# Performance work log

Hardware: AMD Instinct MI355X
Metric: run time of the kernel (lower is better)

## Reference

```python
import jax, jax.numpy as jnp
import numpy as np
import math

SQRT32 = math.sqrt(32.0)


def _l2norm(x, eps=1e-12):
    # matches torch.nn.functional.normalize(dim=-1): x / max(||x||, eps)
    n = jnp.linalg.norm(x, axis=-1, keepdims=True)
    return x / jnp.maximum(n, eps)


def setup_inputs() -> dict:
    key = jax.random.key(0)
    k1, k2 = jax.random.split(key)
    z = jax.random.normal(k1, (8, 256, 32, 32), dtype=jnp.float32)
    # trunc_normal_(std=0.02) init approximated by scaled normal
    embed_weight = jax.random.normal(k2, (16384, 256), dtype=jnp.float32) * 0.02
    return {"z": z, "embed_weight": embed_weight}


def reference(z, embed_weight):
    # z: [b, d, h, w] channel-first -> pack to [b*h*w, d]
    b, d, h, w = z.shape
    zf = jnp.transpose(z, (0, 2, 3, 1)).reshape(-1, d)  # [N, d]

    # l2_norm=True, no predefined codebook: distance = -z @ normalize(E)^T
    ew = _l2norm(embed_weight)                          # [K, d]
    dist = -(zf @ ew.T)                                 # [N, K]
    min_encoding_indices = jnp.argmin(dist, axis=1)     # [N]

    # gather UNnormalized embedding rows, then normalize (as in source)
    z_q = _l2norm(embed_weight[min_encoding_indices])   # [N, d]

    # straight-through estimator
    z_q = zf + jax.lax.stop_gradient(z_q - zf)

    loss = jnp.zeros((1,), dtype=z.dtype)

    # unpack to [b, h, w, d]
    zq_bhwd = z_q.reshape(b, h, w, d)
    # torch .long() truncates toward zero; astype(int) does the same
    bit_indices = (zq_bhwd * SQRT32).astype(jnp.int32) + 4
    zq_out = jnp.transpose(zq_bhwd, (0, 3, 1, 2))       # [b, d, h, w]

    return zq_out, min_encoding_indices, bit_indices, loss
```

## Files before the change

### kernel.cpp

```cpp
#include <hip/hip_runtime.h>
#include <math.h>

#define D      256
#define K      16384
#define NPTS   8192
#define DELTA  0.2f
#define LCAP   1024
#define MAXCAP 4000000u

#define O_IDX  2097152
#define O_BIT  2105344
#define O_LOSS 4202496

typedef __attribute__((ext_vector_type(8))) short bf16x8;
typedef __attribute__((ext_vector_type(4))) float f32x4;
typedef unsigned long long u64;

__device__ __forceinline__ unsigned f2s(float f) {
    unsigned u = __float_as_uint(f);
    return (u & 0x80000000u) ? ~u : (u | 0x80000000u);
}
__device__ __forceinline__ float s2f(unsigned s) {
    return __uint_as_float((s & 0x80000000u) ? (s & 0x7fffffffu) : ~s);
}
__device__ __forceinline__ unsigned short f2bf(float f) {
    unsigned u = __float_as_uint(f);
    u += 0x7fffu + ((u >> 16) & 1u);
    return (unsigned short)(u >> 16);
}


__global__ __launch_bounds__(256) void prep(const float* __restrict__ E,
                                            const float* __restrict__ z,
                                            float* __restrict__ den,
                                            unsigned short* __restrict__ ewbT,
                                            unsigned short* __restrict__ zfbT,
                                            float* __restrict__ zf32,
                                            unsigned* __restrict__ gmax,
                                            u64* __restrict__ keys,
                                            unsigned* __restrict__ cnt) {
    const int blk = blockIdx.x, tid = threadIdx.x;
    if (blk < 512) {
        const int lane = tid & 63, wave = tid >> 6;
        if (blk < 32)        gmax[blk * 256 + tid] = 0u;
        else if (blk < 64)   keys[(blk - 32) * 256 + tid] = 0ull;
        else if (blk == 64 && tid < 2) cnt[tid] = 0u;
        #pragma unroll
        for (int j = 0; j < 8; ++j) {
            const int row = blk * 32 + wave * 8 + j;
            const float4 v = *(const float4*)(E + (size_t)row * D + lane * 4);
            float ss = v.x * v.x + v.y * v.y + v.z * v.z + v.w * v.w;
            #pragma unroll
            for (int o = 1; o < 64; o <<= 1) ss += __shfl_xor(ss, o);
            const float dn = fmaxf(sqrtf(ss), 1e-12f);
            const unsigned lo = (unsigned)f2bf(v.x / dn) | ((unsigned)f2bf(v.y / dn) << 16);
            const unsigned hi = (unsigned)f2bf(v.z / dn) | ((unsigned)f2bf(v.w / dn) << 16);
            *(uint2*)(ewbT + ((size_t)(lane >> 1) * K + row) * 8 + (lane & 1) * 4)
                = make_uint2(lo, hi);
            if (lane == 0) den[row] = dn;
        }
    } else {
        const int bi = blk - 512;
        const int b = bi >> 4, hw0 = (bi & 15) * 64;
        __shared__ float t[64][65];
        for (int dc = 0; dc < D; dc += 64) {
            #pragma unroll
            for (int it = 0; it < 16; ++it) {
                const int idx = it * 256 + tid;
                const int dl = idx >> 6, hw = idx & 63;
                t[dl][hw] = z[(size_t)(b * 256 + dc + dl) * 1024 + hw0 + hw];
            }
            __syncthreads();
            #pragma unroll
            for (int it = 0; it < 16; ++it) {
                const int idx = it * 256 + tid;
                const int pl = idx >> 6, dl = idx & 63;
                const float v = t[dl][pl];
                const int p = b * 1024 + hw0 + pl, k = dc + dl;
                zfbT[((size_t)(k >> 3) * NPTS + p) * 8 + (k & 7)] = f2bf(v);
                zf32[(size_t)p * D + k] = v;
            }
            __syncthreads();
        }
    }
}

#define GEMM_CORE()                                                                 \
    f32x4 acc[4][4];                                                                \
    _Pragma("unroll")                                                               \
    for (int i = 0; i < 4; ++i)                                                     \
        _Pragma("unroll")                                                           \
        for (int j = 0; j < 4; ++j) acc[i][j] = (f32x4){0.f, 0.f, 0.f, 0.f};        \
    {                                                                               \
        const unsigned short* pA = zfbT + ((size_t)quad * NPTS + m0 + wm * 64 + col) * 8; \
        const unsigned short* pB = ewbT + ((size_t)quad * K    + n0 + wn * 64 + col) * 8; \
        _Pragma("unroll")                                                           \
        for (int dc = 0; dc < 8; ++dc) {                                            \
            bf16x8 af[4], bfr[4];                                                   \
            _Pragma("unroll")                                                       \
            for (int mt = 0; mt < 4; ++mt)                                          \
                af[mt] = *(const bf16x8*)(pA + (size_t)dc * 4 * NPTS * 8 + mt * 128);\
            _Pragma("unroll")                                                       \
            for (int nt = 0; nt < 4; ++nt)                                          \
                bfr[nt] = *(const bf16x8*)(pB + (size_t)dc * 4 * K * 8 + nt * 128); \
            _Pragma("unroll")                                                       \
            for (int mt = 0; mt < 4; ++mt)                                          \
                _Pragma("unroll")                                                   \
                for (int nt = 0; nt < 4; ++nt)                                      \
                    acc[mt][nt] = __builtin_amdgcn_mfma_f32_16x16x32_bf16(af[mt], bfr[nt], \
                                                                          acc[mt][nt], 0, 0, 0); \
        }                                                                           \
    }

__global__ __launch_bounds__(256, 3) void score_seed(const unsigned short* __restrict__ zfbT,
                                                     const unsigned short* __restrict__ ewbT,
                                                     unsigned* __restrict__ gmax,
                                                     u64* __restrict__ cand,
                                                     unsigned* __restrict__ cnt,
                                                     unsigned cap) {
    __shared__ unsigned thrS[128];
    __shared__ u64 lbuf[LCAP];
    __shared__ unsigned lcount, lbase;

    const int tid = threadIdx.x, lane = tid & 63, wave = tid >> 6;
    const int quad = lane >> 4, col = lane & 15;
    const int wm = wave >> 1, wn = wave & 1;
    const int m0 = blockIdx.x * 128;
    const int n0 = blockIdx.y * 128;
    const int shsrc = lane & 48;

    if (tid < 128) thrS[tid] = 0u;
    if (tid == 0) lcount = 0u;

    GEMM_CORE()
    __syncthreads();

    float red[4][4];
    #pragma unroll
    for (int mt = 0; mt < 4; ++mt)
        #pragma unroll
        for (int r = 0; r < 4; ++r)
            red[mt][r] = fmaxf(fmaxf(acc[mt][0][r], acc[mt][1][r]),
                               fmaxf(acc[mt][2][r], acc[mt][3][r]));
    #pragma unroll
    for (int off = 1; off < 16; off <<= 1)
        #pragma unroll
        for (int mt = 0; mt < 4; ++mt)
            #pragma unroll
            for (int r = 0; r < 4; ++r)
                red[mt][r] = fmaxf(red[mt][r], __shfl_xor(red[mt][r], off));
    #pragma unroll
    for (int mt = 0; mt < 4; ++mt)
        #pragma unroll
        for (int r = 0; r < 4; ++r) {
            const int pl = wm * 64 + mt * 16 + quad * 4 + r;
            unsigned cur = 0;
            if (col == 0) {
                const unsigned enc = f2s(red[mt][r]);
                const unsigned old = atomicMax(&thrS[pl], enc);
                cur = old > enc ? old : enc;
            }
            cur = (unsigned)__shfl((int)cur, shsrc);
            red[mt][r] = s2f(cur) - DELTA;
        }

    const int ncode0 = n0 + wn * 64 + col;
    #pragma unroll
    for (int mt = 0; mt < 4; ++mt) {
        #pragma unroll
        for (int r = 0; r < 4; ++r) {
            const float tp = red[mt][r];
            const unsigned pt = m0 + wm * 64 + mt * 16 + quad * 4 + r;
            #pragma unroll
            for (int nt = 0; nt < 4; ++nt) {
                const float v = acc[mt][nt][r];
                if (v >= tp) {
                    const unsigned slot = atomicAdd(&lcount, 1u);
                    const u64 e = ((u64)((pt << 14) | (unsigned)(ncode0 + nt * 16)) << 32)
                                  | f2s(v);
                    if (slot < LCAP) lbuf[slot] = e;
                    else {
                        const unsigned g = atomicAdd(cnt, 1u);
                        if (g < cap) cand[g] = e;
                    }
                }
            }
        }
    }

    __syncthreads();
    if (tid < 128) atomicMax(&gmax[m0 + tid], thrS[tid]);
    const unsigned m_ = lcount < LCAP ? lcount : LCAP;
    if (tid == 0) lbase = atomicAdd(cnt, m_);
    __syncthreads();
    for (unsigned i = tid; i < m_; i += 256) {
        const unsigned g = lbase + i;
        if (g < cap) cand[g] = lbuf[i];
    }
}

__global__ __launch_bounds__(256, 3) void score_main(const unsigned short* __restrict__ zfbT,
                                                     const unsigned short* __restrict__ ewbT,
                                                     const unsigned* __restrict__ gmax,
                                                     u64* __restrict__ cand,
                                                     unsigned* __restrict__ cnt,
                                                     unsigned cap) {
    __shared__ float thrL[128];
    __shared__ u64 lbuf[LCAP];
    __shared__ unsigned lcount, lbase;

    const int tid = threadIdx.x, lane = tid & 63, wave = tid >> 6;
    const int quad = lane >> 4, col = lane & 15;
    const int wm = wave >> 1, wn = wave & 1;
    const int m0 = blockIdx.x * 128;
    const int n0 = (16 + blockIdx.y) * 128;

    if (tid < 128) thrL[tid] = s2f(gmax[m0 + tid]) - DELTA;
    if (tid == 0) lcount = 0u;

    GEMM_CORE()
    __syncthreads();

    const int ncode0 = n0 + wn * 64 + col;
    #pragma unroll
    for (int mt = 0; mt < 4; ++mt) {
        #pragma unroll
        for (int r = 0; r < 4; ++r) {
            const int pl = wm * 64 + mt * 16 + quad * 4 + r;
            const float tp = thrL[pl];
            #pragma unroll
            for (int nt = 0; nt < 4; ++nt) {
                const float v = acc[mt][nt][r];
                if (v >= tp) {
                    const unsigned slot = atomicAdd(&lcount, 1u);
                    const u64 e = ((u64)(((unsigned)pl + m0) << 14 | (unsigned)(ncode0 + nt * 16)) << 32)
                                  | f2s(v);
                    if (slot < LCAP) lbuf[slot] = e;
                    else {
                        const unsigned g = atomicAdd(cnt, 1u);
                        if (g < cap) cand[g] = e;
                    }
                }
            }
        }
    }

    __syncthreads();
    const unsigned m_ = lcount < LCAP ? lcount : LCAP;
    if (tid == 0) lbase = atomicAdd(cnt, m_);
    __syncthreads();
    for (unsigned i = tid; i < m_; i += 256) {
        const unsigned g = lbase + i;
        if (g < cap) cand[g] = lbuf[i];
    }
}

__global__ __launch_bounds__(256) void cand_max(const u64* __restrict__ cand,
                                                const unsigned* __restrict__ cnt,
                                                unsigned* __restrict__ gmax,
                                                unsigned cap) {
    const unsigned total = min(cnt[0], cap);
    const unsigned stride = gridDim.x * 256;
    for (unsigned i = blockIdx.x * 256 + threadIdx.x; i < total; i += stride) {
        const u64 e = cand[i];
        atomicMax(&gmax[(unsigned)(e >> 46)], (unsigned)(e & 0xffffffffull));
    }
}

__global__ __launch_bounds__(256) void rescore(const float* __restrict__ zf32,
                                               const float* __restrict__ E,
                                               const float* __restrict__ den,
                                               const unsigned* __restrict__ gmax,
                                               const u64* __restrict__ cand,
                                               const unsigned* __restrict__ cnt,
                                               u64* __restrict__ keys,
                                               unsigned cap) {
    const unsigned total = min(cnt[0], cap);
    const int lane = threadIdx.x & 63;
    const unsigned w = (blockIdx.x * 256 + threadIdx.x) >> 6;
    const unsigned nw = gridDim.x * 4;
    for (unsigned base = w * 64; base < total; base += nw * 64) {
        const unsigned i = base + lane;
        u64 e = 0;
        bool keep = false;
        if (i < total) {
            e = cand[i];
            const int p = (int)(e >> 46);
            keep = (s2f((unsigned)(e & 0xffffffffull)) >= s2f(gmax[p]) - DELTA);
        }
        u64 mask = __ballot(keep);
        while (mask) {
            const int src = __ffsll((long long)mask) - 1;
            mask &= mask - 1;
            const unsigned pc = (unsigned)__shfl((int)(unsigned)(e >> 32), src);
            const int p = pc >> 14, c = pc & 16383;
            const float dinv = 1.0f / den[c];
            const float4 a = *(const float4*)(zf32 + (size_t)p * D + lane * 4);
            const float4 b = *(const float4*)(E + (size_t)c * D + lane * 4);
            float sv = fmaf(a.x, b.x * dinv, fmaf(a.y, b.y * dinv,
                       fmaf(a.z, b.z * dinv, a.w * (b.w * dinv))));
            #pragma unroll
            for (int o = 1; o < 64; o <<= 1) sv += __shfl_xor(sv, o);
            if (lane == 0)
                atomicMax(keys + p, ((u64)f2s(sv) << 32) | (unsigned)(16383 - c));
        }
    }
}

__global__ __launch_bounds__(256) void finalize(const float* __restrict__ E,
                                                const float* __restrict__ den,
                                                const u64* __restrict__ keys,
                                                float* __restrict__ out) {
    __shared__ float t[32][257];
    __shared__ int sIdx[32];
    __shared__ float sDen[32];
    const int tid = threadIdx.x;
    const int n0 = blockIdx.x * 32;
    if (tid < 32) {
        const u64 key = keys[n0 + tid];
        const int idx = 16383 - (int)(unsigned)(key & 0xffffffffull);
        sIdx[tid] = idx;
        sDen[tid] = den[idx];
        out[O_IDX + n0 + tid] = (float)idx;
    }
    __syncthreads();
    const float S = 5.65685424949238019520675489683895f;
    #pragma unroll 4
    for (int i = 0; i < 32; ++i) {
        const float v = E[(size_t)sIdx[i] * D + tid] / sDen[i];
        t[i][tid] = v;
        out[O_BIT + (size_t)(n0 + i) * D + tid] = (float)((int)(v * S) + 4);
    }
    __syncthreads();
    const int b = n0 >> 10, hw0 = n0 & 1023;
    const int hwl = tid & 31, cg = tid >> 5;
    #pragma unroll 4
    for (int cc = 0; cc < 32; ++cc) {
        const int c = cc * 8 + cg;
        out[(size_t)(b * 256 + c) * 1024 + hw0 + hwl] = t[hwl][c];
    }
    if (n0 == 0 && tid == 0) out[O_LOSS] = 0.0f;
}

extern "C" void kernel_launch(void* const* d_in, const int* in_sizes, int n_in,
                              void* d_out, int out_size, void* d_ws, size_t ws_size,
                              hipStream_t stream) {
    const float* z = (const float*)d_in[0];
    const float* E = (const float*)d_in[1];
    float* out = (float*)d_out;

    char* w = (char*)d_ws;
    unsigned short* ewbT = (unsigned short*)w;  w += (size_t)K * D * 2;
    unsigned short* zfbT = (unsigned short*)w;  w += (size_t)NPTS * D * 2;
    float*          zf32 = (float*)w;           w += (size_t)NPTS * D * 4;
    u64*            keys = (u64*)w;             w += (size_t)NPTS * 8;
    float*          den  = (float*)w;           w += (size_t)K * 4;
    unsigned*       gmax = (unsigned*)w;        w += (size_t)NPTS * 4;
    unsigned*       cnt  = (unsigned*)w;        w += 256;
    u64*            cand = (u64*)w;
    const size_t fixed = (size_t)(w - (char*)d_ws);
    const size_t avail = ws_size > fixed ? (ws_size - fixed) / 8 : 0;
    const unsigned cap = (unsigned)(avail < (size_t)MAXCAP ? avail : (size_t)MAXCAP);

    prep<<<640, 256, 0, stream>>>(E, z, den, ewbT, zfbT, zf32, gmax, keys, cnt);

    dim3 gpre(NPTS / 128, 16);
    score_seed<<<gpre, 256, 0, stream>>>(zfbT, ewbT, gmax, cand, cnt, cap);
    dim3 gmain(NPTS / 128, 112);
    score_main<<<gmain, 256, 0, stream>>>(zfbT, ewbT, gmax, cand, cnt, cap);

    cand_max<<<256, 256, 0, stream>>>(cand, cnt, gmax, cap);
    rescore<<<1024, 256, 0, stream>>>(zf32, E, den, gmax, cand, cnt, keys, cap);
    finalize<<<NPTS / 32, 256, 0, stream>>>(E, den, keys, out);
}
```

Before: 264.5 us.

## Stage GEMM operands into swizzled LDS via direct global-to-LDS loads with XCD remap

The score kernels now copy the full 128x256 A and B tiles into LDS with global_load_lds and XOR swizzling, then run the MFMA loop out of LDS instead of loading fragments straight from global memory. Block indices are remapped so each XCD works on a group of row tiles, which should improve L2 reuse. Overflow appends to the candidate buffer are aggregated per wave into one atomic, and prep writes the bf16 transposed z as 16-byte vectors. The 128 KB of LDS per block cuts occupancy to one block per CU, and there is no double buffering, so global-load latency is no longer overlapped.

```diff
diff --git a/kernel.cpp b/kernel.cpp
--- a/kernel.cpp
+++ b/kernel.cpp
@@ -27,6 +27,12 @@
     unsigned u = __float_as_uint(f);
     u += 0x7fffu + ((u >> 16) & 1u);
     return (unsigned short)(u >> 16);
+}
+
+__device__ __forceinline__ void gload16(const unsigned short* g, unsigned short* l) {
+    __builtin_amdgcn_global_load_lds(
+        (const __attribute__((address_space(1))) unsigned int*)g,
+        (__attribute__((address_space(3))) unsigned int*)l, 16, 0, 0);
 }
 
 
@@ -75,49 +81,100 @@
             for (int it = 0; it < 16; ++it) {
                 const int idx = it * 256 + tid;
                 const int pl = idx >> 6, dl = idx & 63;
-                const float v = t[dl][pl];
-                const int p = b * 1024 + hw0 + pl, k = dc + dl;
-                zfbT[((size_t)(k >> 3) * NPTS + p) * 8 + (k & 7)] = f2bf(v);
-                zf32[(size_t)p * D + k] = v;
+                zf32[(size_t)(b * 1024 + hw0 + pl) * D + dc + dl] = t[dl][pl];
+            }
+            #pragma unroll
+            for (int tk = 0; tk < 2; ++tk) {
+                const int task = tk * 256 + tid;
+                const int ch = task >> 6, pl = task & 63;
+                const int p = b * 1024 + hw0 + pl;
+                unsigned short u[8];
+                #pragma unroll
+                for (int j = 0; j < 8; ++j) u[j] = f2bf(t[ch * 8 + j][pl]);
+                *(uint4*)(zfbT + ((size_t)((dc >> 3) + ch) * NPTS + p) * 8) = *(uint4*)u;
             }
             __syncthreads();
         }
     }
 }
+
+
+#define STAGE_ALL()                                                                 \
+    _Pragma("unroll")                                                               \
+    for (int g_ = 0; g_ < 8; ++g_) {                                                \
+        { const int c_ = 4 * g_ + hi_;                                              \
+          gload16(zfbT + ((size_t)c_ * NPTS + m0 + (th_ ^ ((c_ & 3) << 1))) * 8,    \
+                  &sA[c_][th_][0]); }                                               \
+        { const int c_ = 4 * g_ + 2 + hi_;                                          \
+          gload16(zfbT + ((size_t)c_ * NPTS + m0 + (th_ ^ ((c_ & 3) << 1))) * 8,    \
+                  &sA[c_][th_][0]); }                                               \
+        { const int c_ = 4 * g_ + hi_;                                              \
+          gload16(ewbT + ((size_t)c_ * K + n0 + (th_ ^ ((c_ & 3) << 1))) * 8,       \
+                  &sB[c_][th_][0]); }                                               \
+        { const int c_ = 4 * g_ + 2 + hi_;                                          \
+          gload16(ewbT + ((size_t)c_ * K + n0 + (th_ ^ ((c_ & 3) << 1))) * 8,       \
+                  &sB[c_][th_][0]); }                                               \
+    }
 
 #define GEMM_CORE()                                                                 \
     f32x4 acc[4][4];                                                                \
     _Pragma("unroll")                                                               \
-    for (int i = 0; i < 4; ++i)                                                     \
+    for (int i_ = 0; i_ < 4; ++i_)                                                  \
         _Pragma("unroll")                                                           \
-        for (int j = 0; j < 4; ++j) acc[i][j] = (f32x4){0.f, 0.f, 0.f, 0.f};        \
+        for (int j_ = 0; j_ < 4; ++j_) acc[i_][j_] = (f32x4){0.f, 0.f, 0.f, 0.f};   \
     {                                                                               \
-        const unsigned short* pA = zfbT + ((size_t)quad * NPTS + m0 + wm * 64 + col) * 8; \
-        const unsigned short* pB = ewbT + ((size_t)quad * K    + n0 + wn * 64 + col) * 8; \
+        const int th_ = tid & 127, hi_ = tid >> 7;                                  \
+        STAGE_ALL()                                                                 \
+    }                                                                               \
+    __syncthreads();         \
+    {                                                                               \
+        const int rA_ = (wm * 64 + col) ^ (quad << 1);                              \
+        const int rB_ = (wn * 64 + col) ^ (quad << 1);                              \
         _Pragma("unroll")                                                           \
-        for (int dc = 0; dc < 8; ++dc) {                                            \
-            bf16x8 af[4], bfr[4];                                                   \
+        for (int dc_ = 0; dc_ < 8; ++dc_) {                                         \
+            const unsigned short* pa_ = &sA[4 * dc_ + quad][rA_][0];                \
+            const unsigned short* pb_ = &sB[4 * dc_ + quad][rB_][0];                \
+            bf16x8 af_[4], bf_[4];                                                  \
             _Pragma("unroll")                                                       \
-            for (int mt = 0; mt < 4; ++mt)                                          \
-                af[mt] = *(const bf16x8*)(pA + (size_t)dc * 4 * NPTS * 8 + mt * 128);\
+            for (int mt_ = 0; mt_ < 4; ++mt_) {                                     \
+                af_[mt_] = *(const bf16x8*)(pa_ + mt_ * 128);                       \
+                bf_[mt_] = *(const bf16x8*)(pb_ + mt_ * 128);                       \
+            }                                                                       \
             _Pragma("unroll")                                                       \
-            for (int nt = 0; nt < 4; ++nt)                                          \
-                bfr[nt] = *(const bf16x8*)(pB + (size_t)dc * 4 * K * 8 + nt * 128); \
-            _Pragma("unroll")                                                       \
-            for (int mt = 0; mt < 4; ++mt)                                          \
+            for (int mt_ = 0; mt_ < 4; ++mt_)                                       \
                 _Pragma("unroll")                                                   \
-                for (int nt = 0; nt < 4; ++nt)                                      \
-                    acc[mt][nt] = __builtin_amdgcn_mfma_f32_16x16x32_bf16(af[mt], bfr[nt], \
-                                                                          acc[mt][nt], 0, 0, 0); \
+                for (int nt_ = 0; nt_ < 4; ++nt_)                                   \
+                    acc[mt_][nt_] = __builtin_amdgcn_mfma_f32_16x16x32_bf16(        \
+                        af_[mt_], bf_[nt_], acc[mt_][nt_], 0, 0, 0);                \
         }                                                                           \
     }
 
-__global__ __launch_bounds__(256, 3) void score_seed(const unsigned short* __restrict__ zfbT,
+#define CAND_APPEND(e)                                                              \
+    do {                                                                            \
+        const u64 am_ = __builtin_amdgcn_read_exec();                               \
+        const unsigned n_ = (unsigned)__popcll(am_);                                \
+        const unsigned rk_ = (unsigned)__popcll(am_ & ((1ull << lane) - 1));        \
+        unsigned base_ = 0;                                                         \
+        if (rk_ == 0) base_ = atomicAdd(cnt, n_);                                   \
+        base_ = (unsigned)__builtin_amdgcn_readfirstlane((int)base_);               \
+        const unsigned g_ = base_ + rk_;                                            \
+        if (g_ < cap) cand[g_] = (e);                                               \
+    } while (0)
+
+#define XCD_DECODE(NT0)                                                             \
+    const unsigned bid_ = blockIdx.x;                                               \
+    const unsigned j_ = bid_ >> 3;                                                  \
+    const int m0 = (int)(((bid_ & 7u) << 3) | (j_ & 7u)) * 128;                     \
+    const int n0 = ((NT0) + (int)(j_ >> 3)) * 128;
+
+__global__ __launch_bounds__(256, 1) void score_seed(const unsigned short* __restrict__ zfbT,
                                                      const unsigned short* __restrict__ ewbT,
                                                      unsigned* __restrict__ gmax,
                                                      u64* __restrict__ cand,
                                                      unsigned* __restrict__ cnt,
                                                      unsigned cap) {
+    __shared__ unsigned short sA[32][128][8];
+    __shared__ unsigned short sB[32][128][8];
     __shared__ unsigned thrS[128];
     __shared__ u64 lbuf[LCAP];
     __shared__ unsigned lcount, lbase;
@@ -125,15 +182,13 @@
     const int tid = threadIdx.x, lane = tid & 63, wave = tid >> 6;
     const int quad = lane >> 4, col = lane & 15;
     const int wm = wave >> 1, wn = wave & 1;
-    const int m0 = blockIdx.x * 128;
-    const int n0 = blockIdx.y * 128;
+    XCD_DECODE(0)
     const int shsrc = lane & 48;
 
     if (tid < 128) thrS[tid] = 0u;
     if (tid == 0) lcount = 0u;
 
     GEMM_CORE()
-    __syncthreads();
 
     float red[4][4];
     #pragma unroll
@@ -179,10 +234,7 @@
                     const u64 e = ((u64)((pt << 14) | (unsigned)(ncode0 + nt * 16)) << 32)
                                   | f2s(v);
                     if (slot < LCAP) lbuf[slot] = e;
-                    else {
-                        const unsigned g = atomicAdd(cnt, 1u);
-                        if (g < cap) cand[g] = e;
-                    }
+                    else CAND_APPEND(e);
                 }
             }
         }
@@ -199,12 +251,14 @@
     }
 }
 
-__global__ __launch_bounds__(256, 3) void score_main(const unsigned short* __restrict__ zfbT,
+__global__ __launch_bounds__(256, 1) void score_main(const unsigned short* __restrict__ zfbT,
                                                      const unsigned short* __restrict__ ewbT,
                                                      const unsigned* __restrict__ gmax,
                                                      u64* __restrict__ cand,
                                                      unsigned* __restrict__ cnt,
                                                      unsigned cap) {
+    __shared__ unsigned short sA[32][128][8];
+    __shared__ unsigned short sB[32][128][8];
     __shared__ float thrL[128];
     __shared__ u64 lbuf[LCAP];
     __shared__ unsigned lcount, lbase;
@@ -212,14 +266,12 @@
     const int tid = threadIdx.x, lane = tid & 63, wave = tid >> 6;
     const int quad = lane >> 4, col = lane & 15;
     const int wm = wave >> 1, wn = wave & 1;
-    const int m0 = blockIdx.x * 128;
-    const int n0 = (16 + blockIdx.y) * 128;
+    XCD_DECODE(16)
 
     if (tid < 128) thrL[tid] = s2f(gmax[m0 + tid]) - DELTA;
     if (tid == 0) lcount = 0u;
 
     GEMM_CORE()
-    __syncthreads();
 
     const int ncode0 = n0 + wn * 64 + col;
     #pragma unroll
@@ -236,10 +288,7 @@
                     const u64 e = ((u64)(((unsigned)pl + m0) << 14 | (unsigned)(ncode0 + nt * 16)) << 32)
                                   | f2s(v);
                     if (slot < LCAP) lbuf[slot] = e;
-                    else {
-                        const unsigned g = atomicAdd(cnt, 1u);
-                        if (g < cap) cand[g] = e;
-                    }
+                    else CAND_APPEND(e);
                 }
             }
         }
@@ -364,10 +413,8 @@
 
     prep<<<640, 256, 0, stream>>>(E, z, den, ewbT, zfbT, zf32, gmax, keys, cnt);
 
-    dim3 gpre(NPTS / 128, 16);
-    score_seed<<<gpre, 256, 0, stream>>>(zfbT, ewbT, gmax, cand, cnt, cap);
-    dim3 gmain(NPTS / 128, 112);
-    score_main<<<gmain, 256, 0, stream>>>(zfbT, ewbT, gmax, cand, cnt, cap);
+    score_seed<<<1024, 256, 0, stream>>>(zfbT, ewbT, gmax, cand, cnt, cap);
+    score_main<<<7168, 256, 0, stream>>>(zfbT, ewbT, gmax, cand, cnt, cap);
 
     cand_max<<<256, 256, 0, stream>>>(cand, cnt, gmax, cap);
     rescore<<<1024, 256, 0, stream>>>(zf32, E, den, gmax, cand, cnt, keys, cap);
```

Result: slower. 336.8 us (+27.3%).
